# Optimization experiments

Measured on AMD Instinct MI355X. Metric: run time of the kernel, lower is better.

## Reference

```python
import jax, jax.numpy as jnp
import numpy as np

GROUP = 4      # number of groups in the batch dim
SHARED_GP = 4  # conv groups for q/k 1x1 convs
C = 512
N = 4096
B = 4          # B_all = GROUP * B = 16
EPS_LN = 1e-6
EPS_Z = 1e-6


def _phi(x):
    return jax.nn.relu(x) + 1.0


def _grouped_1x1(x, W):
    # x: [B, C, N], W: [g, C/g, C/g] block-diagonal 1x1 conv weights
    Bx, Cx, Nx = x.shape
    g = W.shape[0]
    xg = x.reshape(Bx, g, Cx // g, Nx)
    return jnp.einsum('goc,bgcn->bgon', W, xg).reshape(Bx, Cx, Nx)


def _ln(x, w, b, eps=EPS_LN):
    m = jnp.mean(x, axis=-1, keepdims=True)
    v = jnp.mean(jnp.square(x - m), axis=-1, keepdims=True)
    return (x - m) * jax.lax.rsqrt(v + eps) * w + b


def setup_inputs() -> dict:
    key = jax.random.key(0)
    ks = jax.random.split(key, 12)
    cg = C // SHARED_GP
    s = 1.0 / np.sqrt(C)
    return {
        'x': jax.random.normal(ks[0], (GROUP * B, C, N), dtype=jnp.float32),
        'Wq': jax.random.normal(ks[1], (SHARED_GP, cg, cg), dtype=jnp.float32) / np.sqrt(cg),
        'Wk': jax.random.normal(ks[2], (SHARED_GP, cg, cg), dtype=jnp.float32) / np.sqrt(cg),
        'Wv': jax.random.normal(ks[3], (C, C), dtype=jnp.float32) * s,
        'Wphi': jax.random.normal(ks[4], (C, C), dtype=jnp.float32) * s,
        'ln1_w': jnp.ones((C,), dtype=jnp.float32),
        'ln1_b': jnp.zeros((C,), dtype=jnp.float32),
        'fc1_w': jax.random.normal(ks[5], (4 * C, C), dtype=jnp.float32) * s,
        'fc1_b': jnp.zeros((4 * C,), dtype=jnp.float32),
        'fc2_w': jax.random.normal(ks[6], (C, 4 * C), dtype=jnp.float32) / np.sqrt(4 * C),
        'fc2_b': jnp.zeros((C,), dtype=jnp.float32),
        'ln2_w': jnp.ones((C,), dtype=jnp.float32),
        'ln2_b': jnp.zeros((C,), dtype=jnp.float32),
    }


def reference(x, Wq, Wk, Wv, Wphi, ln1_w, ln1_b, fc1_w, fc1_b, fc2_w, fc2_b, ln2_w, ln2_b):
    B_all, Cc, Nn = x.shape
    g = GROUP
    Bb = B_all // g
    first, rest = x[:Bb], x[Bb:]             # [B,C,N], [M,C,N] with M=(g-1)*B
    M = (g - 1) * Bb

    q = _phi(_grouped_1x1(rest, Wq))          # [M,C,N]
    k0 = _phi(_grouped_1x1(first, Wk))        # [B,C,N]
    v0 = jnp.einsum('oc,bcn->bon', Wv, first)  # [B,C,N]
    phi_first = jnp.einsum('oc,bcn->bon', Wphi, first)
    phi_rest = jnp.einsum('oc,bcn->bon', Wphi, rest)

    # expand first-group k/v across the (g-1) query groups
    k = jnp.broadcast_to(k0[None], (g - 1, Bb, Cc, Nn)).reshape(M, Cc, Nn)
    v = jnp.broadcast_to(v0[None], (g - 1, Bb, Cc, Nn)).reshape(M, Cc, Nn)

    Qg = jnp.broadcast_to(k0.mean(axis=2, keepdims=True)[None],
                          (g - 1, Bb, Cc, 1)).reshape(M, Cc, 1)
    alpha = jax.nn.softmax(jnp.sum(Qg * k, axis=1, keepdims=True), axis=-1) * Nn  # [M,1,N]
    k_hat = k * alpha

    # linear attention: kv = k_hat @ v^T / sqrt(C)
    kv = jnp.einsum('mcn,mdn->mcd', k_hat, v) / jnp.sqrt(jnp.asarray(Cc, x.dtype))  # [M,C,C]
    k_sum = jnp.sum(k_hat, axis=-1)                                  # [M,C]
    z = 1.0 / (jnp.einsum('mcn,mc->mn', q, k_sum)[:, None, :] + EPS_Z)  # [M,1,N]
    y = jnp.einsum('mcn,mcd->mdn', q, kv) * z * phi_rest              # [M,C,N]

    y_first = jnp.mean(y, axis=0, keepdims=True) * phi_first          # [B,C,N]
    out_first = _ln((first + y_first).transpose(0, 2, 1), ln1_w, ln1_b)  # [B,N,C]
    h = jax.nn.relu(out_first @ fc1_w.T + fc1_b)
    out_first = out_first + h @ fc2_w.T + fc2_b
    out_first = jax.nn.relu(_ln(out_first, ln2_w, ln2_b))
    out_first = out_first.transpose(0, 2, 1)                          # [B,C,N]
    return jnp.concatenate([out_first, rest], axis=0)
```

## Files before the change

kernel.cpp:

```cpp
#include <hip/hip_runtime.h>

#define N_DIM 4096
#define C_DIM 512
#define CN_ ((long)C_DIM * (long)N_DIM)

typedef unsigned short ushort_t;
typedef __attribute__((ext_vector_type(8))) short bf16x8;
typedef __attribute__((ext_vector_type(4))) float f32x4;

typedef const __attribute__((address_space(1))) unsigned int* gas_t;
typedef __attribute__((address_space(3))) unsigned int* las_t;
#define GLOAD(g, l) __builtin_amdgcn_global_load_lds((gas_t)(g), (las_t)(l), 16, 0, 0)

__device__ __forceinline__ ushort_t f2b(float f) {
    unsigned u = __builtin_bit_cast(unsigned, f);
    u += 0x7fffu + ((u >> 16) & 1u);
    return (ushort_t)(u >> 16);
}
__device__ __forceinline__ float b2f(ushort_t s) {
    return __builtin_bit_cast(float, (unsigned)s << 16);
}

enum { EPI_NONE = 0, EPI_PHI = 1, EPI_RELU_BIAS = 2, EPI_RES_BIAS = 3, EPI_PRE = 4 };

#define STAGE(q, koff) { \
    GLOAD(ap0 + (koff), &Als[q][la0]); \
    GLOAD(ap1 + (koff), &Als[q][la1]); \
    GLOAD(bp0 + (koff), &Bls[q][la0]); \
    GLOAD(bp1 + (koff), &Bls[q][la1]); }

#define COMPUTE(q) { \
    bf16x8 af[4], bfv[4]; \
    _Pragma("unroll") for (int m_ = 0; m_ < 4; ++m_) \
        af[m_] = *(const bf16x8*)&Als[q][(wr + m_ * 16 + fr) * 32 + rsw]; \
    _Pragma("unroll") for (int nf_ = 0; nf_ < 4; ++nf_) \
        bfv[nf_] = *(const bf16x8*)&Bls[q][(wc + nf_ * 16 + fr) * 32 + rsw]; \
    _Pragma("unroll") for (int m_ = 0; m_ < 4; ++m_) \
        _Pragma("unroll") for (int nf_ = 0; nf_ < 4; ++nf_) \
            acc[m_][nf_] = __builtin_amdgcn_mfma_f32_16x16x32_bf16( \
                af[m_], bfv[nf_], acc[m_][nf_], 0, 0, 0); }

#define KLOOP(K_) { \
    STAGE(0, 0); \
    __syncthreads(); \
    int kk_ = 0; \
    while (true) { \
        if (kk_ + 32 < (K_)) STAGE(1, kk_ + 32); \
        COMPUTE(0); \
        __syncthreads(); \
        kk_ += 32; \
        if (kk_ >= (K_)) break; \
        if (kk_ + 32 < (K_)) STAGE(0, kk_ + 32); \
        COMPUTE(1); \
        __syncthreads(); \
        kk_ += 32; \
        if (kk_ >= (K_)) break; \
    } }

template<int EPI, bool GROUPED, bool OBF, bool DEN>
__global__ __launch_bounds__(256, 3) void mfma_gemm(
    const ushort_t* __restrict__ Wb, const ushort_t* __restrict__ A,
    void* __restrict__ OUTV, const float* __restrict__ bias,
    const ushort_t* __restrict__ auxb, const float* __restrict__ auxf,
    int K, int O, int a_rstride, long a_zstride, long o_zstride, long auxb_zstride,
    int xt, int yt)
{
    __shared__ ushort_t Als[2][128 * 32];
    __shared__ ushort_t Bls[2][128 * 32];
    const int tid = threadIdx.x;

    const int L = blockIdx.x;
    const int gpx = (gridDim.x >> 3) / xt;
    const int xcd = L & 7;
    const int j = L >> 3;
    const int xtile = j % xt;
    const int g = xcd * gpx + j / xt;
    const int ytile = g % yt;
    const int z = g / yt;

    const int o0 = xtile * 128;
    const int n0 = ytile * 128;
    const ushort_t* Az = A + (long)z * a_zstride;
    const ushort_t* Wp = Wb;
    int kbase = 0, obase = o0;
    if (GROUPED) { int gg = o0 >> 7; Wp = Wb + (long)gg * (128 * 128); kbase = gg << 7; obase = 0; }

    const int w = tid >> 6, l = tid & 63;
    const int lr = l >> 2, lg = l & 3;
    const int rA0 = w * 32 + lr, rA1 = w * 32 + 16 + lr;
    const int gA0 = lg ^ ((rA0 >> 1) & 3), gA1 = lg ^ ((rA1 >> 1) & 3);
    const ushort_t* ap0 = Az + (long)(n0 + rA0) * a_rstride + kbase + gA0 * 8;
    const ushort_t* ap1 = Az + (long)(n0 + rA1) * a_rstride + kbase + gA1 * 8;
    const ushort_t* bp0 = Wp + (long)(obase + rA0) * K + gA0 * 8;
    const ushort_t* bp1 = Wp + (long)(obase + rA1) * K + gA1 * 8;
    const int la0 = (w * 32) * 32, la1 = (w * 32 + 16) * 32;

    const int wr = (w >> 1) * 64, wc = (w & 1) * 64;
    const int fr = l & 15, ks = l >> 4;
    const int rsw = (ks ^ ((fr >> 1) & 3)) << 3;

    f32x4 acc[4][4];
#pragma unroll
    for (int m = 0; m < 4; ++m)
#pragma unroll
        for (int nf = 0; nf < 4; ++nf) acc[m][nf] = f32x4{0.f, 0.f, 0.f, 0.f};

    KLOOP(K);

    float dsum[4][4];
    if (DEN) {
#pragma unroll
        for (int m = 0; m < 4; ++m)
#pragma unroll
            for (int j2 = 0; j2 < 4; ++j2) dsum[m][j2] = 0.f;
    }

#pragma unroll
    for (int m = 0; m < 4; ++m) {
#pragma unroll
        for (int nf = 0; nf < 4; ++nf) {
            const int oo = o0 + wc + nf * 16 + fr;
            float bval = 0.f;
            if (EPI == EPI_RELU_BIAS || EPI == EPI_RES_BIAS) bval = bias[oo];
            float kw = 0.f;
            if (DEN) kw = bias[((z & 3) << 9) + oo];
#pragma unroll
            for (int j2 = 0; j2 < 4; ++j2) {
                const int nn = n0 + wr + m * 16 + ks * 4 + j2;
                const long ridx = (long)nn * O + oo;
                float v = acc[m][nf][j2];
                if (EPI == EPI_PHI)            v = fmaxf(v, 0.f) + 1.f;
                else if (EPI == EPI_RELU_BIAS) v = fmaxf(v + bval, 0.f);
                else if (EPI == EPI_RES_BIAS)  v = v + bval + b2f(auxb[(long)z * auxb_zstride + ridx]);
                else if (EPI == EPI_PRE)       v = b2f(auxb[(long)z * auxb_zstride + ridx]) + auxf[ridx] * v;
                if (DEN) dsum[m][j2] += v * kw;
                if (OBF) ((ushort_t*)OUTV)[(long)z * o_zstride + ridx] = f2b(v);
                else     ((float*)OUTV)[(long)z * o_zstride + ridx] = v;
            }
        }
    }

    if (DEN) {
#pragma unroll
        for (int m = 0; m < 4; ++m)
#pragma unroll
            for (int j2 = 0; j2 < 4; ++j2) {
                float d = dsum[m][j2];
                d += __shfl_xor(d, 1); d += __shfl_xor(d, 2);
                d += __shfl_xor(d, 4); d += __shfl_xor(d, 8);
                if (fr == 0) {
                    const int nn = n0 + wr + m * 16 + ks * 4 + j2;
                    atomicAdd((float*)&auxf[(long)z * N_DIM + nn], d);
                }
            }
    }
}

__global__ __launch_bounds__(256, 3) void kv_mfma(
    const ushort_t* __restrict__ v0c, const ushort_t* __restrict__ khat,
    float* __restrict__ kvb)
{
    __shared__ ushort_t Als[2][128 * 32];
    __shared__ ushort_t Bls[2][128 * 32];
    const int tid = threadIdx.x;
    const int L = blockIdx.x;
    const int gpx = (gridDim.x >> 3) >> 2;
    const int xcd = L & 7;
    const int j = L >> 3;
    const int xtile = j & 3;
    const int g = xcd * gpx + (j >> 2);
    const int ytile = g & 3;
    const int z = g >> 2;
    const int c0 = xtile * 128, d0 = ytile * 128;
    const int b = z >> 3, nch = z & 7;

    const int w = tid >> 6, l = tid & 63;
    const int lr = l >> 2, lg = l & 3;
    const int rA0 = w * 32 + lr, rA1 = w * 32 + 16 + lr;
    const int gA0 = lg ^ ((rA0 >> 1) & 3), gA1 = lg ^ ((rA1 >> 1) & 3);
    const ushort_t* Ab = v0c + (long)b * CN_ + nch * 512;
    const ushort_t* Bb = khat + (long)b * CN_ + nch * 512;
    const ushort_t* ap0 = Ab + (long)(d0 + rA0) * N_DIM + gA0 * 8;
    const ushort_t* ap1 = Ab + (long)(d0 + rA1) * N_DIM + gA1 * 8;
    const ushort_t* bp0 = Bb + (long)(c0 + rA0) * N_DIM + gA0 * 8;
    const ushort_t* bp1 = Bb + (long)(c0 + rA1) * N_DIM + gA1 * 8;
    const int la0 = (w * 32) * 32, la1 = (w * 32 + 16) * 32;

    const int wr = (w >> 1) * 64, wc = (w & 1) * 64;
    const int fr = l & 15, ks = l >> 4;
    const int rsw = (ks ^ ((fr >> 1) & 3)) << 3;

    f32x4 acc[4][4];
#pragma unroll
    for (int m = 0; m < 4; ++m)
#pragma unroll
        for (int nf = 0; nf < 4; ++nf) acc[m][nf] = f32x4{0.f, 0.f, 0.f, 0.f};

    KLOOP(512);

    float* KV = kvb + (long)b * 262144;
#pragma unroll
    for (int m = 0; m < 4; ++m)
#pragma unroll
        for (int nf = 0; nf < 4; ++nf) {
            const int cc = c0 + wc + nf * 16 + fr;
#pragma unroll
            for (int j2 = 0; j2 < 4; ++j2) {
                const int dd = d0 + wr + m * 16 + ks * 4 + j2;
                atomicAdd(&KV[(long)dd * 512 + cc], acc[m][nf][j2]);
            }
        }
}

__global__ __launch_bounds__(256, 3) void ybar_gemm(
    const ushort_t* __restrict__ q12, const ushort_t* __restrict__ kvT,
    const ushort_t* __restrict__ phi12, const float* __restrict__ den12,
    ushort_t* __restrict__ y12)
{
    __shared__ ushort_t Als[2][128 * 32];
    __shared__ ushort_t Bls[2][128 * 32];
    const int tid = threadIdx.x;
    const int L = blockIdx.x;
    const int gpx = (gridDim.x >> 3) >> 2;
    const int xcd = L & 7;
    const int j = L >> 3;
    const int xtile = j & 3;
    const int g = xcd * gpx + (j >> 2);
    const int ytile = g & 31;
    const int mm = g >> 5;
    const int o0 = xtile * 128, n0 = ytile * 128;

    const int w = tid >> 6, l = tid & 63;
    const int lr = l >> 2, lg = l & 3;
    const int rA0 = w * 32 + lr, rA1 = w * 32 + 16 + lr;
    const int gA0 = lg ^ ((rA0 >> 1) & 3), gA1 = lg ^ ((rA1 >> 1) & 3);
    const ushort_t* ap0 = q12 + (long)mm * CN_ + (long)(n0 + rA0) * 512 + gA0 * 8;
    const ushort_t* ap1 = q12 + (long)mm * CN_ + (long)(n0 + rA1) * 512 + gA1 * 8;
    const ushort_t* bp0 = kvT + (long)(mm & 3) * 262144 + (long)(o0 + rA0) * 512 + gA0 * 8;
    const ushort_t* bp1 = kvT + (long)(mm & 3) * 262144 + (long)(o0 + rA1) * 512 + gA1 * 8;
    const int la0 = (w * 32) * 32, la1 = (w * 32 + 16) * 32;

    const int wr = (w >> 1) * 64, wc = (w & 1) * 64;
    const int fr = l & 15, ks = l >> 4;
    const int rsw = (ks ^ ((fr >> 1) & 3)) << 3;

    f32x4 acc[4][4];
#pragma unroll
    for (int m = 0; m < 4; ++m)
#pragma unroll
        for (int nf = 0; nf < 4; ++nf) acc[m][nf] = f32x4{0.f, 0.f, 0.f, 0.f};

    KLOOP(512);

    const ushort_t* P = phi12 + (long)mm * CN_;
    const float* D = den12 + (long)mm * N_DIM;
    ushort_t* Y = y12 + (long)mm * CN_;
#pragma unroll
    for (int m = 0; m < 4; ++m) {
        float zr[4];
#pragma unroll
        for (int j2 = 0; j2 < 4; ++j2)
            zr[j2] = 1.f / (D[n0 + wr + m * 16 + ks * 4 + j2] + 1e-6f);
#pragma unroll
        for (int nf = 0; nf < 4; ++nf) {
            const int oo = o0 + wc + nf * 16 + fr;
#pragma unroll
            for (int j2 = 0; j2 < 4; ++j2) {
                const int nn = n0 + wr + m * 16 + ks * 4 + j2;
                const long idx = (long)nn * 512 + oo;
                Y[idx] = f2b(acc[m][nf][j2] * zr[j2] * b2f(P[idx]));
            }
        }
    }
}

__global__ __launch_bounds__(256) void ybar_reduce(
    const ushort_t* __restrict__ y12, float* __restrict__ ybar)
{
    const long i = ((long)blockIdx.x * 256 + threadIdx.x) * 8;
    float s[8] = {0.f, 0.f, 0.f, 0.f, 0.f, 0.f, 0.f, 0.f};
    for (int mm = 0; mm < 12; ++mm) {
        uint4 u = *(const uint4*)&y12[(long)mm * CN_ + i];
        const ushort_t* us = (const ushort_t*)&u;
#pragma unroll
        for (int j = 0; j < 8; ++j) s[j] += b2f(us[j]);
    }
#pragma unroll
    for (int j = 0; j < 8; ++j) s[j] *= (1.f / 12.f);
    *(float4*)&ybar[i] = make_float4(s[0], s[1], s[2], s[3]);
    *(float4*)&ybar[i + 4] = make_float4(s[4], s[5], s[6], s[7]);
}

__global__ __launch_bounds__(256) void cvt_scale(
    const float* __restrict__ in, ushort_t* __restrict__ out)
{
    const float s = 0.044194173824159216f;
    int i = (blockIdx.x * 256 + threadIdx.x) * 4;
    float4 v = *(const float4*)&in[i];
    union { ushort_t sh[4]; uint2 u; } p;
    p.sh[0] = f2b(v.x * s); p.sh[1] = f2b(v.y * s);
    p.sh[2] = f2b(v.z * s); p.sh[3] = f2b(v.w * s);
    *(uint2*)&out[i] = p.u;
}

template<int ALPHA>
__global__ __launch_bounds__(256) void transpose_b2b(
    const ushort_t* __restrict__ in, ushort_t* __restrict__ out,
    const float* __restrict__ alpha)
{
    __shared__ ushort_t t[64][72];
    const int tid = threadIdx.x;
    const int n0 = blockIdx.x * 64, c0 = blockIdx.y * 64, z = blockIdx.z;
    const ushort_t* I = in + (long)z * CN_;
    ushort_t* O = out + (long)z * CN_;
    const int r = tid >> 2, s8 = (tid & 3) * 16;
    uint4 u0 = *(const uint4*)&I[(long)(n0 + r) * 512 + c0 + s8];
    uint4 u1 = *(const uint4*)&I[(long)(n0 + r) * 512 + c0 + s8 + 8];
    *(uint4*)&t[r][s8] = u0;
    *(uint4*)&t[r][s8 + 8] = u1;
    __syncthreads();
    union { ushort_t sh[16]; uint4 u[2]; } p;
#pragma unroll
    for (int i = 0; i < 16; ++i) {
        ushort_t v = t[s8 + i][r];
        if (ALPHA) v = f2b(b2f(v) * alpha[(long)z * N_DIM + n0 + s8 + i]);
        p.sh[i] = v;
    }
    uint4* dst = (uint4*)&O[(long)(c0 + r) * N_DIM + n0 + s8];
    dst[0] = p.u[0]; dst[1] = p.u[1];
}

__global__ __launch_bounds__(256) void cvt_all(
    const float* __restrict__ s0, ushort_t* __restrict__ d0,
    const float* __restrict__ s1, ushort_t* __restrict__ d1,
    const float* __restrict__ s2, ushort_t* __restrict__ d2,
    const float* __restrict__ s3, ushort_t* __restrict__ d3,
    const float* __restrict__ s4, ushort_t* __restrict__ d4,
    const float* __restrict__ s5, ushort_t* __restrict__ d5)
{
    long i = ((long)blockIdx.x * 256 + threadIdx.x) * 4;
    const float* s; ushort_t* d; long off;
    if (i < 65536)        { s = s0; d = d0; off = i; }
    else if (i < 131072)  { s = s1; d = d1; off = i - 65536; }
    else if (i < 393216)  { s = s2; d = d2; off = i - 131072; }
    else if (i < 655360)  { s = s3; d = d3; off = i - 393216; }
    else if (i < 1703936) { s = s4; d = d4; off = i - 655360; }
    else                  { s = s5; d = d5; off = i - 1703936; }
    float4 v = *(const float4*)&s[off];
    union { ushort_t sh[4]; uint2 u; } p;
    p.sh[0] = f2b(v.x); p.sh[1] = f2b(v.y); p.sh[2] = f2b(v.z); p.sh[3] = f2b(v.w);
    *(uint2*)&d[off] = p.u;
}

__global__ __launch_bounds__(256) void transpose_f2b(
    const float* __restrict__ in, ushort_t* __restrict__ out,
    int rows, int cols, long in_z, long out_z)
{
    __shared__ float t[64][65];
    const int tid = threadIdx.x;
    const int n0 = blockIdx.x * 64, c0 = blockIdx.y * 64;
    const float* I = in + (long)blockIdx.z * in_z;
    ushort_t* Ot = out + (long)blockIdx.z * out_z;
    const int r = tid >> 2, s4 = (tid & 3) * 16;
#pragma unroll
    for (int i = 0; i < 16; i += 4) {
        float4 v = *(const float4*)&I[(long)(c0 + r) * cols + n0 + s4 + i];
        t[r][s4 + i] = v.x; t[r][s4 + i + 1] = v.y;
        t[r][s4 + i + 2] = v.z; t[r][s4 + i + 3] = v.w;
    }
    __syncthreads();
    union { ushort_t s[16]; uint4 u[2]; } pk;
#pragma unroll
    for (int i = 0; i < 16; ++i) pk.s[i] = f2b(t[s4 + i][r]);
    uint4* dst = (uint4*)&Ot[(long)(n0 + r) * rows + c0 + s4];
    dst[0] = pk.u[0]; dst[1] = pk.u[1];
}

__global__ __launch_bounds__(256) void colreduce_part(
    const ushort_t* __restrict__ X, const float* __restrict__ wgt,
    float* __restrict__ part)
{
    const int ns = blockIdx.x, b = blockIdx.y;
    const int tid = threadIdx.x;
    const int w = tid >> 6, l = tid & 63;
    const int c8 = l * 8;
    const ushort_t* Xb = X + (long)b * CN_;
    float acc[8] = {0.f, 0.f, 0.f, 0.f, 0.f, 0.f, 0.f, 0.f};
    for (int r = w; r < 128; r += 4) {
        const int n = ns * 128 + r;
        uint4 u = *(const uint4*)&Xb[(long)n * C_DIM + c8];
        const ushort_t* us = (const ushort_t*)&u;
        const float wv = wgt ? wgt[(long)b * N_DIM + n] : 1.f;
#pragma unroll
        for (int i = 0; i < 8; ++i) acc[i] += b2f(us[i]) * wv;
    }
    __shared__ float red[4][512];
#pragma unroll
    for (int i = 0; i < 8; ++i) red[w][c8 + i] = acc[i];
    __syncthreads();
    for (int c = tid; c < 512; c += 256) {
        part[((long)ns * 4 + b) * C_DIM + c] =
            red[0][c] + red[1][c] + red[2][c] + red[3][c];
    }
}

__global__ __launch_bounds__(256) void colreduce_fin(
    const float* __restrict__ part, float* __restrict__ out, float scale)
{
    int b = blockIdx.x;
    for (int c = threadIdx.x; c < 512; c += 256) {
        float s = 0.f;
        for (int ns = 0; ns < 32; ++ns) s += part[((long)ns * 4 + b) * C_DIM + c];
        out[b * C_DIM + c] = s * scale;
    }
}

__global__ __launch_bounds__(256) void dot_rows(
    const ushort_t* __restrict__ X, const float* __restrict__ w,
    float* __restrict__ out)
{
    const int tid = threadIdx.x;
    const int rn = tid >> 2, cs = (tid & 3) * 128;
    const int z = blockIdx.y;
    const int n = blockIdx.x * 64 + rn;
    const ushort_t* row = X + (long)z * CN_ + (long)n * C_DIM;
    const float* wz = w + (long)(z & 3) * C_DIM;
    float s = 0.f;
    for (int i = 0; i < 128; i += 8) {
        uint4 u = *(const uint4*)&row[cs + i];
        const ushort_t* us = (const ushort_t*)&u;
#pragma unroll
        for (int k2 = 0; k2 < 8; ++k2) s += b2f(us[k2]) * wz[cs + i + k2];
    }
    s += __shfl_xor(s, 1); s += __shfl_xor(s, 2);
    if ((tid & 3) == 0) out[(long)z * N_DIM + n] = s;
}

__global__ __launch_bounds__(256) void softmax_alpha(
    const float* __restrict__ logits, float* __restrict__ alpha)
{
    int b = blockIdx.x, tid = threadIdx.x;
    const float* L = logits + (long)b * N_DIM;
    float* A = alpha + (long)b * N_DIM;
    float lv[16];
    float mx = -3.4e38f;
#pragma unroll
    for (int i = 0; i < 4; i++) {
        float4 v = *(const float4*)&L[tid * 4 + i * 1024];
        lv[4 * i + 0] = v.x; lv[4 * i + 1] = v.y; lv[4 * i + 2] = v.z; lv[4 * i + 3] = v.w;
        mx = fmaxf(mx, fmaxf(fmaxf(v.x, v.y), fmaxf(v.z, v.w)));
    }
    __shared__ float red[8];
    float m = mx;
#pragma unroll
    for (int off = 32; off; off >>= 1) m = fmaxf(m, __shfl_down(m, off, 64));
    int wid = tid >> 6, lane = tid & 63;
    if (lane == 0) red[wid] = m;
    __syncthreads();
    m = fmaxf(fmaxf(red[0], red[1]), fmaxf(red[2], red[3]));
    float e[16], s = 0.f;
#pragma unroll
    for (int i = 0; i < 16; i++) { e[i] = expf(lv[i] - m); s += e[i]; }
#pragma unroll
    for (int off = 32; off; off >>= 1) s += __shfl_down(s, off, 64);
    if (lane == 0) red[4 + wid] = s;
    __syncthreads();
    float S = red[4] + red[5] + red[6] + red[7];
    float sc = 4096.f / S;
#pragma unroll
    for (int i = 0; i < 4; i++)
        *(float4*)&A[tid * 4 + i * 1024] =
            make_float4(e[4 * i] * sc, e[4 * i + 1] * sc, e[4 * i + 2] * sc, e[4 * i + 3] * sc);
}

template<int RELU, int OBF, int IBF>
__global__ __launch_bounds__(256) void ln_row(
    const void* __restrict__ inv, const float* __restrict__ g,
    const float* __restrict__ bt, void* __restrict__ outv)
{
    const int tid = threadIdx.x;
    const int r = tid >> 3, cs = (tid & 7) * 64;
    const long base = (((long)blockIdx.y * N_DIM) + blockIdx.x * 32 + r) * C_DIM + cs;
    float vv[64];
    float s = 0.f, s2 = 0.f;
    if (IBF) {
        const ushort_t* I = (const ushort_t*)inv + base;
#pragma unroll
        for (int i = 0; i < 8; ++i) {
            uint4 u = *(const uint4*)&I[i * 8];
            const ushort_t* us = (const ushort_t*)&u;
#pragma unroll
            for (int jj = 0; jj < 8; ++jj) {
                float f = b2f(us[jj]); vv[i * 8 + jj] = f; s += f; s2 += f * f;
            }
        }
    } else {
        const float* I = (const float*)inv + base;
#pragma unroll
        for (int i = 0; i < 16; ++i) {
            float4 v = *(const float4*)&I[i * 4];
            vv[i * 4] = v.x; vv[i * 4 + 1] = v.y; vv[i * 4 + 2] = v.z; vv[i * 4 + 3] = v.w;
            s += v.x + v.y + v.z + v.w;
            s2 += v.x * v.x + v.y * v.y + v.z * v.z + v.w * v.w;
        }
    }
#pragma unroll
    for (int off = 1; off < 8; off <<= 1) { s += __shfl_xor(s, off); s2 += __shfl_xor(s2, off); }
    const float mean = s * (1.f / 512.f);
    const float var = s2 * (1.f / 512.f) - mean * mean;
    const float rs = rsqrtf(var + 1e-6f);
#pragma unroll
    for (int i = 0; i < 64; i += 4) {
        float o[4];
#pragma unroll
        for (int jj = 0; jj < 4; ++jj) {
            float ov = (vv[i + jj] - mean) * rs * g[cs + i + jj] + bt[cs + i + jj];
            if (RELU) ov = fmaxf(ov, 0.f);
            o[jj] = ov;
        }
        if (OBF) {
            union { ushort_t s4[4]; uint2 u; } p;
            p.s4[0] = f2b(o[0]); p.s4[1] = f2b(o[1]); p.s4[2] = f2b(o[2]); p.s4[3] = f2b(o[3]);
            *(uint2*)&((ushort_t*)outv)[base + i] = p.u;
        } else {
            *(float4*)&((float*)outv)[base + i] = make_float4(o[0], o[1], o[2], o[3]);
        }
    }
}

__global__ __launch_bounds__(256) void ln_tr(
    const ushort_t* __restrict__ in, const float* __restrict__ g,
    const float* __restrict__ bt, float* __restrict__ out)
{
    __shared__ float t[32][513];
    const int tid = threadIdx.x;
    const int r = tid >> 3;
    const int lc = (tid & 7) * 8;
    const int z = blockIdx.y;
    const long n = (long)blockIdx.x * 32 + r;
    const ushort_t* I = in + ((long)z * N_DIM + n) * C_DIM;
    float vv[64];
    float s = 0.f, s2 = 0.f;
#pragma unroll
    for (int i = 0; i < 8; ++i) {
        const int c = i * 64 + lc;
        uint4 u = *(const uint4*)&I[c];
        const ushort_t* us = (const ushort_t*)&u;
#pragma unroll
        for (int jj = 0; jj < 8; ++jj) {
            float f = b2f(us[jj]); vv[i * 8 + jj] = f; s += f; s2 += f * f;
        }
    }
#pragma unroll
    for (int off = 1; off < 8; off <<= 1) { s += __shfl_xor(s, off); s2 += __shfl_xor(s2, off); }
    const float mean = s * (1.f / 512.f);
    const float var = s2 * (1.f / 512.f) - mean * mean;
    const float rs = rsqrtf(var + 1e-6f);
#pragma unroll
    for (int i = 0; i < 8; ++i) {
        const int c = i * 64 + lc;
#pragma unroll
        for (int jj = 0; jj < 8; ++jj) {
            float o = (vv[i * 8 + jj] - mean) * rs * g[c + jj] + bt[c + jj];
            t[r][c + jj] = fmaxf(o, 0.f);
        }
    }
    __syncthreads();
    float* O = out + (long)z * CN_ + (long)blockIdx.x * 32;
    for (int c = tid; c < 512; c += 256) {
        float* dst = O + (long)c * N_DIM;
#pragma unroll
        for (int i = 0; i < 32; i += 4)
            *(float4*)&dst[i] = make_float4(t[i][c], t[i + 1][c], t[i + 2][c], t[i + 3][c]);
    }
}

extern "C" void kernel_launch(void* const* d_in, const int* in_sizes, int n_in,
                              void* d_out, int out_size, void* d_ws, size_t ws_size,
                              hipStream_t stream)
{
    const float* x     = (const float*)d_in[0];
    const float* Wq    = (const float*)d_in[1];
    const float* Wk    = (const float*)d_in[2];
    const float* Wv    = (const float*)d_in[3];
    const float* Wphi  = (const float*)d_in[4];
    const float* ln1_w = (const float*)d_in[5];
    const float* ln1_b = (const float*)d_in[6];
    const float* fc1_w = (const float*)d_in[7];
    const float* fc1_bias = (const float*)d_in[8];
    const float* fc2_w = (const float*)d_in[9];
    const float* fc2_bias = (const float*)d_in[10];
    const float* ln2_w = (const float*)d_in[11];
    const float* ln2_b = (const float*)d_in[12];
    float* out = (float*)d_out;

    float* ws = (float*)d_ws;
    const long CN = CN_;
    ushort_t* xTfirst = (ushort_t*)ws;
    ushort_t* tln     = (ushort_t*)ws;
    ushort_t* xT12 = (ushort_t*)(ws + 2 * CN);
    ushort_t* hbuf4 = (ushort_t*)(ws + 2 * CN);
    ushort_t* q12   = (ushort_t*)(ws + 8 * CN);
    ushort_t* phi12 = (ushort_t*)(ws + 14 * CN);
    ushort_t* k0b = (ushort_t*)(ws + 20 * CN);
    ushort_t* v0b = (ushort_t*)(ws + 22 * CN);
    ushort_t* y12 = (ushort_t*)(ws + 20 * CN);
    ushort_t* pre_b = (ushort_t*)(ws + 20 * CN);
    ushort_t* khat = (ushort_t*)(ws + 24 * CN);
    ushort_t* v0c  = (ushort_t*)(ws + 26 * CN);
    ushort_t* ubuf_b = (ushort_t*)(ws + 24 * CN);
    float* ybar = ws + 32 * CN;
    float* kvb  = ws + 33 * CN;
    ushort_t* kvT = (ushort_t*)(ws + 33 * CN + 1048576);
    float* wb = ws + 33 * CN + 1572864;
    ushort_t* Wk_b   = (ushort_t*)(wb);
    ushort_t* Wq_b   = (ushort_t*)(wb + 32768);
    ushort_t* Wv_b   = (ushort_t*)(wb + 65536);
    ushort_t* Wphi_b = (ushort_t*)(wb + 196608);
    ushort_t* fc1_b16 = (ushort_t*)(wb + 327680);
    ushort_t* fc2_b16 = (ushort_t*)(wb + 851968);
    float* part   = wb + 1376256;
    float* Qg     = wb + 1441792;
    float* ksum   = wb + 1443840;
    float* logits = wb + 1445888;
    float* alpha  = wb + 1462272;
    float* den12  = wb + 1478656;

    dim3 blk(256);

    cvt_all<<<2688, blk, 0, stream>>>(Wk, Wk_b, Wq, Wq_b, Wv, Wv_b,
                                      Wphi, Wphi_b, fc1_w, fc1_b16, fc2_w, fc2_b16);
    hipMemsetAsync(kvb, 0, 1048576 * sizeof(float), stream);
    hipMemsetAsync(den12, 0, 49152 * sizeof(float), stream);

    transpose_f2b<<<dim3(64, 8, 16), blk, 0, stream>>>(x, xTfirst, 512, 4096, CN, CN);

    mfma_gemm<EPI_PHI, true, true, false><<<512, blk, 0, stream>>>(
        Wk_b, xTfirst, k0b, nullptr, nullptr, nullptr, 128, 512, 512, CN, CN, 0, 4, 32);
    mfma_gemm<EPI_NONE, false, true, false><<<512, blk, 0, stream>>>(
        Wv_b, xTfirst, v0b, nullptr, nullptr, nullptr, 512, 512, 512, CN, CN, 0, 4, 32);
    colreduce_part<<<dim3(32, 4), blk, 0, stream>>>(k0b, nullptr, part);
    colreduce_fin<<<4, blk, 0, stream>>>(part, Qg, 1.f / 4096.f);
    dot_rows<<<dim3(64, 4), blk, 0, stream>>>(k0b, Qg, logits);
    softmax_alpha<<<4, blk, 0, stream>>>(logits, alpha);
    colreduce_part<<<dim3(32, 4), blk, 0, stream>>>(k0b, alpha, part);
    colreduce_fin<<<4, blk, 0, stream>>>(part, ksum, 1.f);
    transpose_b2b<1><<<dim3(64, 8, 4), blk, 0, stream>>>(k0b, khat, alpha);
    transpose_b2b<0><<<dim3(64, 8, 4), blk, 0, stream>>>(v0b, v0c, nullptr);
    kv_mfma<<<512, blk, 0, stream>>>(v0c, khat, kvb);
    cvt_scale<<<1024, blk, 0, stream>>>(kvb, kvT);

    mfma_gemm<EPI_PHI, true, true, true><<<1536, blk, 0, stream>>>(
        Wq_b, xT12, q12, ksum, nullptr, den12, 128, 512, 512, CN, CN, 0, 4, 32);
    mfma_gemm<EPI_NONE, false, true, false><<<1536, blk, 0, stream>>>(
        Wphi_b, xT12, phi12, nullptr, nullptr, nullptr, 512, 512, 512, CN, CN, 0, 4, 32);
    ybar_gemm<<<1536, blk, 0, stream>>>(q12, kvT, phi12, den12, y12);
    ybar_reduce<<<1024, blk, 0, stream>>>(y12, ybar);

    mfma_gemm<EPI_PRE, false, true, false><<<512, blk, 0, stream>>>(
        Wphi_b, xTfirst, pre_b, nullptr, xTfirst, ybar, 512, 512, 512, CN, CN, CN, 4, 32);
    ln_row<0, 1, 1><<<dim3(128, 4), blk, 0, stream>>>(pre_b, ln1_w, ln1_b, tln);
    mfma_gemm<EPI_RELU_BIAS, false, true, false><<<2048, blk, 0, stream>>>(
        fc1_b16, tln, hbuf4, fc1_bias, nullptr, nullptr,
        512, 2048, 512, CN, 8388608, 0, 16, 32);
    mfma_gemm<EPI_RES_BIAS, false, true, false><<<512, blk, 0, stream>>>(
        fc2_b16, hbuf4, ubuf_b, fc2_bias, tln, nullptr,
        2048, 512, 2048, 8388608, CN, CN, 4, 32);
    ln_tr<<<dim3(128, 4), blk, 0, stream>>>(ubuf_b, ln2_w, ln2_b, out);

    hipMemcpyAsync(out + 4 * CN, x + 4 * CN, 12 * CN * sizeof(float),
                   hipMemcpyDeviceToDevice, stream);
}
```

Baseline: 511.2 us.

## Fuse phi_rest GEMM into ybar GEMM and fold passthrough copy into transpose

The ybar kernel now runs two K-loops per tile. The first computes the Wphi projection of the rest batches and keeps it in registers as packed bf16, and the second computes q@kv and scales by it. This removes a separate GEMM launch and the write and re-read of the phi12 buffer (12 x C x N bf16). The input transpose also writes the untouched rest batches straight to the output while it already holds them, which replaces the trailing device-to-device memcpy. In exchange, register pressure rises, occupancy drops from 3 to 2 blocks per CU, and the transpose does extra stores.

```diff
diff --git a/kernel.cpp b/kernel.cpp
--- a/kernel.cpp
+++ b/kernel.cpp
@@ -212,10 +212,10 @@
         }
 }
 
-__global__ __launch_bounds__(256, 3) void ybar_gemm(
+__global__ __launch_bounds__(256, 2) void ybar_gemm(
     const ushort_t* __restrict__ q12, const ushort_t* __restrict__ kvT,
-    const ushort_t* __restrict__ phi12, const float* __restrict__ den12,
-    ushort_t* __restrict__ y12)
+    const ushort_t* __restrict__ xT12, const ushort_t* __restrict__ Wphi_b,
+    const float* __restrict__ den12, ushort_t* __restrict__ y12)
 {
     __shared__ ushort_t Als[2][128 * 32];
     __shared__ ushort_t Bls[2][128 * 32];
@@ -234,10 +234,10 @@
     const int lr = l >> 2, lg = l & 3;
     const int rA0 = w * 32 + lr, rA1 = w * 32 + 16 + lr;
     const int gA0 = lg ^ ((rA0 >> 1) & 3), gA1 = lg ^ ((rA1 >> 1) & 3);
-    const ushort_t* ap0 = q12 + (long)mm * CN_ + (long)(n0 + rA0) * 512 + gA0 * 8;
-    const ushort_t* ap1 = q12 + (long)mm * CN_ + (long)(n0 + rA1) * 512 + gA1 * 8;
-    const ushort_t* bp0 = kvT + (long)(mm & 3) * 262144 + (long)(o0 + rA0) * 512 + gA0 * 8;
-    const ushort_t* bp1 = kvT + (long)(mm & 3) * 262144 + (long)(o0 + rA1) * 512 + gA1 * 8;
+    const long aoff0 = (long)(n0 + rA0) * 512 + gA0 * 8;
+    const long aoff1 = (long)(n0 + rA1) * 512 + gA1 * 8;
+    const long boff0 = (long)(o0 + rA0) * 512 + gA0 * 8;
+    const long boff1 = (long)(o0 + rA1) * 512 + gA1 * 8;
     const int la0 = (w * 32) * 32, la1 = (w * 32 + 16) * 32;
 
     const int wr = (w >> 1) * 64, wc = (w & 1) * 64;
@@ -250,9 +250,28 @@
 #pragma unroll
         for (int nf = 0; nf < 4; ++nf) acc[m][nf] = f32x4{0.f, 0.f, 0.f, 0.f};
 
+    const ushort_t* ap0 = xT12 + (long)mm * CN_ + aoff0;
+    const ushort_t* ap1 = xT12 + (long)mm * CN_ + aoff1;
+    const ushort_t* bp0 = Wphi_b + boff0;
+    const ushort_t* bp1 = Wphi_b + boff1;
     KLOOP(512);
 
-    const ushort_t* P = phi12 + (long)mm * CN_;
+    uint2 ph[4][4];
+#pragma unroll
+    for (int m = 0; m < 4; ++m)
+#pragma unroll
+        for (int nf = 0; nf < 4; ++nf) {
+            ph[m][nf].x = (unsigned)f2b(acc[m][nf][0]) | ((unsigned)f2b(acc[m][nf][1]) << 16);
+            ph[m][nf].y = (unsigned)f2b(acc[m][nf][2]) | ((unsigned)f2b(acc[m][nf][3]) << 16);
+            acc[m][nf] = f32x4{0.f, 0.f, 0.f, 0.f};
+        }
+
+    ap0 = q12 + (long)mm * CN_ + aoff0;
+    ap1 = q12 + (long)mm * CN_ + aoff1;
+    bp0 = kvT + (long)(mm & 3) * 262144 + boff0;
+    bp1 = kvT + (long)(mm & 3) * 262144 + boff1;
+    KLOOP(512);
+
     const float* D = den12 + (long)mm * N_DIM;
     ushort_t* Y = y12 + (long)mm * CN_;
 #pragma unroll
@@ -264,11 +283,15 @@
 #pragma unroll
         for (int nf = 0; nf < 4; ++nf) {
             const int oo = o0 + wc + nf * 16 + fr;
+            float pv[4];
+            pv[0] = b2f((ushort_t)(ph[m][nf].x & 0xffff));
+            pv[1] = b2f((ushort_t)(ph[m][nf].x >> 16));
+            pv[2] = b2f((ushort_t)(ph[m][nf].y & 0xffff));
+            pv[3] = b2f((ushort_t)(ph[m][nf].y >> 16));
 #pragma unroll
             for (int j2 = 0; j2 < 4; ++j2) {
                 const int nn = n0 + wr + m * 16 + ks * 4 + j2;
-                const long idx = (long)nn * 512 + oo;
-                Y[idx] = f2b(acc[m][nf][j2] * zr[j2] * b2f(P[idx]));
+                Y[(long)nn * 512 + oo] = f2b(acc[m][nf][j2] * zr[j2] * pv[j2]);
             }
         }
     }
@@ -352,21 +375,30 @@
     *(uint2*)&d[off] = p.u;
 }
 
+template<int PASSZ>
 __global__ __launch_bounds__(256) void transpose_f2b(
     const float* __restrict__ in, ushort_t* __restrict__ out,
-    int rows, int cols, long in_z, long out_z)
+    int rows, int cols, long in_z, long out_z, float* __restrict__ passout)
 {
     __shared__ float t[64][65];
     const int tid = threadIdx.x;
     const int n0 = blockIdx.x * 64, c0 = blockIdx.y * 64;
-    const float* I = in + (long)blockIdx.z * in_z;
-    ushort_t* Ot = out + (long)blockIdx.z * out_z;
+    const int z = blockIdx.z;
+    const float* I = in + (long)z * in_z;
+    ushort_t* Ot = out + (long)z * out_z;
     const int r = tid >> 2, s4 = (tid & 3) * 16;
+    float4 raw[4];
 #pragma unroll
     for (int i = 0; i < 16; i += 4) {
         float4 v = *(const float4*)&I[(long)(c0 + r) * cols + n0 + s4 + i];
+        raw[i >> 2] = v;
         t[r][s4 + i] = v.x; t[r][s4 + i + 1] = v.y;
         t[r][s4 + i + 2] = v.z; t[r][s4 + i + 3] = v.w;
+    }
+    if (PASSZ && z >= 4) {
+        float* P = passout + (long)z * in_z + (long)(c0 + r) * cols + n0 + s4;
+#pragma unroll
+        for (int i = 0; i < 4; ++i) *(float4*)&P[i * 4] = raw[i];
     }
     __syncthreads();
     union { ushort_t s[16]; uint4 u[2]; } pk;
@@ -601,10 +633,9 @@
     ushort_t* xT12 = (ushort_t*)(ws + 2 * CN);
     ushort_t* hbuf4 = (ushort_t*)(ws + 2 * CN);
     ushort_t* q12   = (ushort_t*)(ws + 8 * CN);
-    ushort_t* phi12 = (ushort_t*)(ws + 14 * CN);
+    ushort_t* y12   = (ushort_t*)(ws + 14 * CN);
     ushort_t* k0b = (ushort_t*)(ws + 20 * CN);
     ushort_t* v0b = (ushort_t*)(ws + 22 * CN);
-    ushort_t* y12 = (ushort_t*)(ws + 20 * CN);
     ushort_t* pre_b = (ushort_t*)(ws + 20 * CN);
     ushort_t* khat = (ushort_t*)(ws + 24 * CN);
     ushort_t* v0c  = (ushort_t*)(ws + 26 * CN);
@@ -633,7 +664,8 @@
     hipMemsetAsync(kvb, 0, 1048576 * sizeof(float), stream);
     hipMemsetAsync(den12, 0, 49152 * sizeof(float), stream);
 
-    transpose_f2b<<<dim3(64, 8, 16), blk, 0, stream>>>(x, xTfirst, 512, 4096, CN, CN);
+    transpose_f2b<1><<<dim3(64, 8, 16), blk, 0, stream>>>(
+        x, xTfirst, 512, 4096, CN, CN, out);
 
     mfma_gemm<EPI_PHI, true, true, false><<<512, blk, 0, stream>>>(
         Wk_b, xTfirst, k0b, nullptr, nullptr, nullptr, 128, 512, 512, CN, CN, 0, 4, 32);
@@ -652,9 +684,7 @@
 
     mfma_gemm<EPI_PHI, true, true, true><<<1536, blk, 0, stream>>>(
         Wq_b, xT12, q12, ksum, nullptr, den12, 128, 512, 512, CN, CN, 0, 4, 32);
-    mfma_gemm<EPI_NONE, false, true, false><<<1536, blk, 0, stream>>>(
-        Wphi_b, xT12, phi12, nullptr, nullptr, nullptr, 512, 512, 512, CN, CN, 0, 4, 32);
-    ybar_gemm<<<1536, blk, 0, stream>>>(q12, kvT, phi12, den12, y12);
+    ybar_gemm<<<1536, blk, 0, stream>>>(q12, kvT, xT12, Wphi_b, den12, y12);
     ybar_reduce<<<1024, blk, 0, stream>>>(y12, ybar);
 
     mfma_gemm<EPI_PRE, false, true, false><<<512, blk, 0, stream>>>(
@@ -667,7 +697,4 @@
         fc2_b16, hbuf4, ubuf_b, fc2_bias, tln, nullptr,
         2048, 512, 2048, 8388608, CN, CN, 4, 32);
     ln_tr<<<dim3(128, 4), blk, 0, stream>>>(ubuf_b, ln2_w, ln2_b, out);
-
-    hipMemcpyAsync(out + 4 * CN, x + 4 * CN, 12 * CN * sizeof(float),
-                   hipMemcpyDeviceToDevice, stream);
-}
+}
```

Measured after the change: 497.0 us. 1.03x faster.
